# Optimization experiments

Measured on AMD Instinct MI355X. Metric: run time of the kernel, lower is better.

## Reference

```python
import jax, jax.numpy as jnp
import numpy as np

GAMMA = 0.9
TEMPERATURE = 0.07
BASE_TEMPERATURE = 0.07
U_SIZE = 15_000_000
BSZ, N_VIEWS, DIM = 2048, 2, 256


def setup_inputs() -> dict:
    key = jax.random.key(0)
    kf, = jax.random.split(key, 1)
    feats = jax.random.normal(kf, (BSZ, N_VIEWS, DIM), dtype=jnp.float32)
    # contrastive features are unit-normalized in practice
    feats = feats / jnp.linalg.norm(feats, axis=-1, keepdims=True)
    index = jnp.arange(BSZ, dtype=jnp.int64) if jax.config.jax_enable_x64 else jnp.arange(BSZ, dtype=jnp.int32)
    u = jnp.zeros((U_SIZE, 1), dtype=jnp.float32)
    return {"index": index, "features": feats, "u": u}


def reference(index, features, u):
    B, V, D = features.shape          # bsz, n_views, dim
    N = B * V
    eye_b = jnp.eye(B, dtype=jnp.float32)

    # torch.cat(torch.unbind(features, dim=1), dim=0) -> [V*B, D], views stacked
    contrast_feature = jnp.transpose(features, (1, 0, 2)).reshape(N, D)
    anchor_feature = contrast_feature  # contrast_mode == 'all'

    # [N, N] similarity logits
    anchor_dot_contrast = jnp.matmul(anchor_feature, contrast_feature.T) / TEMPERATURE
    logits_max = jax.lax.stop_gradient(jnp.max(anchor_dot_contrast, axis=1, keepdims=True))
    logits = anchor_dot_contrast - logits_max

    # positive mask: tiled identity with self-contrast removed
    mask = jnp.tile(eye_b, (V, V))
    logits_mask = 1.0 - jnp.eye(N, dtype=jnp.float32)  # scatter of zeros on the diagonal
    pos_mask = mask * logits_mask
    neg_mask = 1.0 - pos_mask

    # detached negative exp-logits (EMA statistics)
    neg_exp_logits = jax.lax.stop_gradient(jnp.exp(logits) * neg_mask)

    # indexed EMA buffer update: u[index] = (1-g)*u[index] + g*rowsum[:B]
    row_sum = jnp.sum(neg_exp_logits, axis=1, keepdims=True)[:B]   # [B, 1]
    u_new = (1.0 - GAMMA) * u[index] + GAMMA * row_sum             # [B, 1]
    # (buffer write: u = u.at[index].set(u_new); only u_new is read below)

    p_neg_pairs = neg_exp_logits / jnp.tile(u_new, (V, 1))         # [N, N], detached numer/denom
    log_prob = logits - jnp.sum(p_neg_pairs * logits * neg_mask, axis=1, keepdims=True)

    mean_log_prob_pos = jnp.sum(pos_mask * log_prob, axis=1) / jnp.sum(pos_mask, axis=1)
    loss = -(TEMPERATURE / BASE_TEMPERATURE) * mean_log_prob_pos
    return loss.reshape(V, B).mean()
```

## Files before the change

kernel.cpp:

```cpp
#include <hip/hip_runtime.h>


#define BSZ   2048
#define NROW  4096
#define DDIM  256
#define NB64  64
#define NT2   (NB64 * (NB64 + 1) / 2)
#define C1    (1.4426950408889634f / 0.07f)
#define LN2   0.6931471805599453f

typedef __attribute__((ext_vector_type(8))) __bf16 bf16x8;
typedef __attribute__((ext_vector_type(4))) float f32x4;

__device__ __forceinline__ short f2bs(float x) {
    __bf16 b = (__bf16)x;
    return __builtin_bit_cast(short, b);
}

__device__ __forceinline__ const float* crow_ptr(const float* feats, int i) {
    return feats + (((i & (BSZ - 1)) * 2 + (i >> 11)) << 8);
}

__global__ __launch_bounds__(256) void prep_kernel(const float* __restrict__ feats,
        float* __restrict__ Szero, short* __restrict__ CmF) {
    int gid = blockIdx.x * 256 + threadIdx.x;
    if (gid < 2 * NROW) Szero[gid] = 0.0f;

    int quad = gid & 3;
    int l15  = (gid >> 2) & 15;
    int rt   = (gid >> 6) & 3;
    int k    = (gid >> 8) & 7;
    int b    = gid >> 12;
    int srow = (b << 6) + (rt << 4) + l15;
    int kel  = (k << 5) + (quad << 3);
    const float4* fp = (const float4*)(crow_ptr(feats, srow) + kel);
    float4 v0 = fp[0], v1 = fp[1];
    short h[8] = { f2bs(v0.x), f2bs(v0.y), f2bs(v0.z), f2bs(v0.w),
                   f2bs(v1.x), f2bs(v1.y), f2bs(v1.z), f2bs(v1.w) };
    *(int4*)(CmF + gid * 8) = *(int4*)h;
}

__global__ __launch_bounds__(64, 3) void gemm_sym(const short* __restrict__ CmF,
        float* __restrict__ S1, float* __restrict__ S2,
        float* __restrict__ Praw, float* __restrict__ Draw) {
    int lane = threadIdx.x;
    int quad = lane >> 4;
    int l15  = lane & 15;

    int t = blockIdx.x;
    int p = (int)((sqrtf(8.0f * (float)t + 1.0f) - 1.0f) * 0.5f);
    while ((p + 1) * (p + 2) / 2 <= t) ++p;
    while (p * (p + 1) / 2 > t) --p;
    int q = t - p * (p + 1) / 2;
    int rowBase = q << 6;
    int colBase = p << 6;
    bool offdiag = (p != q);

    int laneOff = ((l15 << 2) + quad) * 8;
    int aO = q * 16384 + laneOff;
    int bO = p * 16384 + laneOff;

    f32x4 acc[4][4];
    #pragma unroll
    for (int a = 0; a < 4; ++a)
        #pragma unroll
        for (int c = 0; c < 4; ++c) acc[a][c] = (f32x4){0.f, 0.f, 0.f, 0.f};

    bf16x8 aF[2][4], bF[2][4];
    #pragma unroll
    for (int rt = 0; rt < 4; ++rt) {
        aF[0][rt] = *(const bf16x8*)(CmF + aO + rt * 512);
        bF[0][rt] = *(const bf16x8*)(CmF + bO + rt * 512);
    }

    #pragma unroll
    for (int k = 0; k < 8; ++k) {
        int cur = k & 1;
        int nxt = cur ^ 1;
        if (k < 7) {
            #pragma unroll
            for (int rt = 0; rt < 4; ++rt) {
                aF[nxt][rt] = *(const bf16x8*)(CmF + aO + ((k + 1) * 4 + rt) * 512);
                bF[nxt][rt] = *(const bf16x8*)(CmF + bO + ((k + 1) * 4 + rt) * 512);
            }
        }
        __builtin_amdgcn_s_setprio(1);
        #pragma unroll
        for (int rt = 0; rt < 4; ++rt)
            #pragma unroll
            for (int ct = 0; ct < 4; ++ct)
                acc[rt][ct] = __builtin_amdgcn_mfma_f32_16x16x32_bf16(
                    aF[cur][rt], bF[cur][ct], acc[rt][ct], 0, 0, 0);
        __builtin_amdgcn_s_setprio(0);
    }

    float S1r[4][4] = {}, S2r[4][4] = {};
    float S1c[4] = {}, S2c[4] = {};
    #pragma unroll
    for (int rt = 0; rt < 4; ++rt) {
        #pragma unroll
        for (int ct = 0; ct < 4; ++ct) {
            #pragma unroll
            for (int r = 0; r < 4; ++r) {
                float d  = acc[rt][ct][r];
                float t0 = d * C1;
                float f  = __builtin_exp2f(t0);
                S1r[rt][r] += f;
                S2r[rt][r] = __builtin_fmaf(f, t0, S2r[rt][r]);
                if (offdiag) {
                    S1c[ct] += f;
                    S2c[ct] = __builtin_fmaf(f, t0, S2c[ct]);
                }
            }
        }
    }

    if (p == (q ^ 32)) {
        if (quad == (l15 >> 2)) {
            int r = l15 & 3;
            #pragma unroll
            for (int rt = 0; rt < 4; ++rt) {
                float t0 = acc[rt][rt][r] * C1;
                Praw[rowBase + rt * 16 + l15] = t0;
                Praw[colBase + rt * 16 + l15] = t0;
            }
        }
    }
    if (!offdiag) {
        if (quad == (l15 >> 2)) {
            int r = l15 & 3;
            #pragma unroll
            for (int rt = 0; rt < 4; ++rt)
                Draw[rowBase + rt * 16 + l15] = acc[rt][rt][r] * C1;
        }
    }

    #pragma unroll
    for (int rt = 0; rt < 4; ++rt) {
        #pragma unroll
        for (int r = 0; r < 4; ++r) {
            float e = S1r[rt][r], w = S2r[rt][r];
            #pragma unroll
            for (int off = 1; off < 16; off <<= 1) {
                e += __shfl_xor(e, off, 64);
                w += __shfl_xor(w, off, 64);
            }
            if (l15 == 0) {
                int grow = rowBase + rt * 16 + (quad << 2) + r;
                atomicAdd(&S1[grow], e);
                atomicAdd(&S2[grow], w);
            }
        }
    }
    if (offdiag) {
        #pragma unroll
        for (int ct = 0; ct < 4; ++ct) {
            float e = S1c[ct], w = S2c[ct];
            e += __shfl_xor(e, 16, 64);  w += __shfl_xor(w, 16, 64);
            e += __shfl_xor(e, 32, 64);  w += __shfl_xor(w, 32, 64);
            if (quad == 0) {
                int gcol = colBase + ct * 16 + l15;
                atomicAdd(&S1[gcol], e);
                atomicAdd(&S2[gcol], w);
            }
        }
    }
}

__global__ __launch_bounds__(1024) void finalize_kernel(const int* __restrict__ index,
        const float* __restrict__ u, const float* __restrict__ S1,
        const float* __restrict__ S2, const float* __restrict__ Praw,
        const float* __restrict__ Draw, float* __restrict__ out) {
    __shared__ float unew[BSZ];
    __shared__ float partial[16];
    int tid = threadIdx.x;
    for (int b = tid; b < BSZ; b += 1024) {
        float m  = -Draw[b];
        float tp = Praw[b] + m;
        float E  = __builtin_exp2f(m) * S1[b];
        unew[b] = 0.1f * u[index[b]] + 0.9f * (E - __builtin_exp2f(tp));
    }
    __syncthreads();
    float local = 0.0f;
    for (int i = tid; i < NROW; i += 1024) {
        float m   = -Draw[i];
        float tp  = Praw[i] + m;
        float etp = __builtin_exp2f(tp);
        float W   = __builtin_exp2f(m) * __builtin_fmaf(m, S1[i], S2[i]);
        local += tp - (W - etp * tp) / unew[i & (BSZ - 1)];
    }
    #pragma unroll
    for (int off = 32; off; off >>= 1) local += __shfl_xor(local, off, 64);
    if ((tid & 63) == 0) partial[tid >> 6] = local;
    __syncthreads();
    if (tid == 0) {
        float s = 0.0f;
        #pragma unroll
        for (int w = 0; w < 16; ++w) s += partial[w];
        out[0] = -LN2 * s / (float)NROW;
    }
}

extern "C" void kernel_launch(void* const* d_in, const int* in_sizes, int n_in,
                              void* d_out, int out_size, void* d_ws, size_t ws_size,
                              hipStream_t stream) {
    const int*   index = (const int*)d_in[0];
    const float* feats = (const float*)d_in[1];
    const float* u     = (const float*)d_in[2];
    float* out = (float*)d_out;

    float* S1   = (float*)d_ws;
    float* S2   = S1 + NROW;
    float* Praw = S2 + NROW;
    float* Draw = Praw + NROW;
    short* CmF  = (short*)((char*)d_ws + 131072);

    prep_kernel<<<1024, 256, 0, stream>>>(feats, S1, CmF);
    gemm_sym<<<NT2, 64, 0, stream>>>(CmF, S1, S2, Praw, Draw);
    finalize_kernel<<<1, 1024, 0, stream>>>(index, u, S1, S2, Praw, Draw, out);
}
```

Before: 114.2 us.

## Triple-buffer GEMM fragment loads and parallelize finalize across blocks with atomics

The symmetric GEMM now prefetches two k-steps ahead with a three-slot register buffer instead of double buffering, and its launch-bounds occupancy hint drops from 3 to 2 to make room for the extra registers. The single-block 1024-thread finalize is replaced by 32 blocks of one wavefront each. Each block handles 64 paired rows and atomically adds into the output, which the prep kernel now zeroes. This aims to hide global load latency in the GEMM and shorten the serial finalize tail, at the cost of lower occupancy and a non-deterministic float atomic reduction order.

New measurement: 111.3 us, median of 2. 1.03x faster.

```diff
diff --git a/kernel.cpp b/kernel.cpp
--- a/kernel.cpp
+++ b/kernel.cpp
@@ -3,7 +3,6 @@
 
 #define BSZ   2048
 #define NROW  4096
-#define DDIM  256
 #define NB64  64
 #define NT2   (NB64 * (NB64 + 1) / 2)
 #define C1    (1.4426950408889634f / 0.07f)
@@ -21,11 +20,8 @@
     return feats + (((i & (BSZ - 1)) * 2 + (i >> 11)) << 8);
 }
 
-__global__ __launch_bounds__(256) void prep_kernel(const float* __restrict__ feats,
-        float* __restrict__ Szero, short* __restrict__ CmF) {
-    int gid = blockIdx.x * 256 + threadIdx.x;
-    if (gid < 2 * NROW) Szero[gid] = 0.0f;
-
+__device__ __forceinline__ void pack_unit(const float* __restrict__ feats,
+                                          short* __restrict__ CmF, int gid) {
     int quad = gid & 3;
     int l15  = (gid >> 2) & 15;
     int rt   = (gid >> 6) & 3;
@@ -40,7 +36,15 @@
     *(int4*)(CmF + gid * 8) = *(int4*)h;
 }
 
-__global__ __launch_bounds__(64, 3) void gemm_sym(const short* __restrict__ CmF,
+__global__ __launch_bounds__(256) void prep_kernel(const float* __restrict__ feats,
+        float* __restrict__ S1, short* __restrict__ CmF, float* __restrict__ out) {
+    int gid = blockIdx.x * 256 + threadIdx.x;
+    if (gid < 2 * NROW) S1[gid] = 0.0f;
+    else if (gid == 2 * NROW) out[0] = 0.0f;
+    pack_unit(feats, CmF, gid);
+}
+
+__global__ __launch_bounds__(64, 2) void gemm_sym(const short* __restrict__ CmF,
         float* __restrict__ S1, float* __restrict__ S2,
         float* __restrict__ Praw, float* __restrict__ Draw) {
     int lane = threadIdx.x;
@@ -57,8 +61,8 @@
     bool offdiag = (p != q);
 
     int laneOff = ((l15 << 2) + quad) * 8;
-    int aO = q * 16384 + laneOff;
-    int bO = p * 16384 + laneOff;
+    const short* aB = CmF + q * 16384 + laneOff;
+    const short* bB = CmF + p * 16384 + laneOff;
 
     f32x4 acc[4][4];
     #pragma unroll
@@ -66,22 +70,27 @@
         #pragma unroll
         for (int c = 0; c < 4; ++c) acc[a][c] = (f32x4){0.f, 0.f, 0.f, 0.f};
 
-    bf16x8 aF[2][4], bF[2][4];
-    #pragma unroll
-    for (int rt = 0; rt < 4; ++rt) {
-        aF[0][rt] = *(const bf16x8*)(CmF + aO + rt * 512);
-        bF[0][rt] = *(const bf16x8*)(CmF + bO + rt * 512);
+    bf16x8 aF[3][4], bF[3][4];
+    #pragma unroll
+    for (int rt = 0; rt < 4; ++rt) {
+        aF[0][rt] = *(const bf16x8*)(aB + (0 * 4 + rt) * 512);
+        bF[0][rt] = *(const bf16x8*)(bB + (0 * 4 + rt) * 512);
+    }
+    #pragma unroll
+    for (int rt = 0; rt < 4; ++rt) {
+        aF[1][rt] = *(const bf16x8*)(aB + (1 * 4 + rt) * 512);
+        bF[1][rt] = *(const bf16x8*)(bB + (1 * 4 + rt) * 512);
     }
 
     #pragma unroll
     for (int k = 0; k < 8; ++k) {
-        int cur = k & 1;
-        int nxt = cur ^ 1;
-        if (k < 7) {
+        int cur = k % 3;
+        int nxt = (k + 2) % 3;
+        if (k < 6) {
             #pragma unroll
             for (int rt = 0; rt < 4; ++rt) {
-                aF[nxt][rt] = *(const bf16x8*)(CmF + aO + ((k + 1) * 4 + rt) * 512);
-                bF[nxt][rt] = *(const bf16x8*)(CmF + bO + ((k + 1) * 4 + rt) * 512);
+                aF[nxt][rt] = *(const bf16x8*)(aB + ((k + 2) * 4 + rt) * 512);
+                bF[nxt][rt] = *(const bf16x8*)(bB + ((k + 2) * 4 + rt) * 512);
             }
         }
         __builtin_amdgcn_s_setprio(1);
@@ -115,24 +124,20 @@
         }
     }
 
-    if (p == (q ^ 32)) {
-        if (quad == (l15 >> 2)) {
-            int r = l15 & 3;
-            #pragma unroll
-            for (int rt = 0; rt < 4; ++rt) {
-                float t0 = acc[rt][rt][r] * C1;
-                Praw[rowBase + rt * 16 + l15] = t0;
-                Praw[colBase + rt * 16 + l15] = t0;
-            }
-        }
-    }
-    if (!offdiag) {
-        if (quad == (l15 >> 2)) {
-            int r = l15 & 3;
-            #pragma unroll
-            for (int rt = 0; rt < 4; ++rt)
-                Draw[rowBase + rt * 16 + l15] = acc[rt][rt][r] * C1;
-        }
+    if (p == (q ^ 32) && quad == (l15 >> 2)) {
+        int r = l15 & 3;
+        #pragma unroll
+        for (int rt = 0; rt < 4; ++rt) {
+            float t0 = acc[rt][rt][r] * C1;
+            Praw[rowBase + rt * 16 + l15] = t0;
+            Praw[colBase + rt * 16 + l15] = t0;
+        }
+    }
+    if (!offdiag && quad == (l15 >> 2)) {
+        int r = l15 & 3;
+        #pragma unroll
+        for (int rt = 0; rt < 4; ++rt)
+            Draw[rowBase + rt * 16 + l15] = acc[rt][rt][r] * C1;
     }
 
     #pragma unroll
@@ -167,38 +172,28 @@
     }
 }
 
-__global__ __launch_bounds__(1024) void finalize_kernel(const int* __restrict__ index,
+__global__ __launch_bounds__(64) void finalize_kernel(const int* __restrict__ index,
         const float* __restrict__ u, const float* __restrict__ S1,
         const float* __restrict__ S2, const float* __restrict__ Praw,
         const float* __restrict__ Draw, float* __restrict__ out) {
-    __shared__ float unew[BSZ];
-    __shared__ float partial[16];
-    int tid = threadIdx.x;
-    for (int b = tid; b < BSZ; b += 1024) {
-        float m  = -Draw[b];
-        float tp = Praw[b] + m;
-        float E  = __builtin_exp2f(m) * S1[b];
-        unew[b] = 0.1f * u[index[b]] + 0.9f * (E - __builtin_exp2f(tp));
-    }
-    __syncthreads();
-    float local = 0.0f;
-    for (int i = tid; i < NROW; i += 1024) {
-        float m   = -Draw[i];
-        float tp  = Praw[i] + m;
-        float etp = __builtin_exp2f(tp);
-        float W   = __builtin_exp2f(m) * __builtin_fmaf(m, S1[i], S2[i]);
-        local += tp - (W - etp * tp) / unew[i & (BSZ - 1)];
-    }
+    int lane = threadIdx.x;
+    int rlo  = (blockIdx.x << 6) + lane;
+    int rhi  = rlo + BSZ;
+
+    float mlo = -Draw[rlo], mhi = -Draw[rhi];
+    float tplo = Praw[rlo] + mlo, tphi = Praw[rhi] + mhi;
+    float Elo  = __builtin_exp2f(mlo) * S1[rlo];
+    float unew = 0.1f * u[index[rlo]] + 0.9f * (Elo - __builtin_exp2f(tplo));
+
+    float Wlo = __builtin_exp2f(mlo) * __builtin_fmaf(mlo, S1[rlo], S2[rlo]);
+    float Whi = __builtin_exp2f(mhi) * __builtin_fmaf(mhi, S1[rhi], S2[rhi]);
+    float etplo = __builtin_exp2f(tplo);
+    float etphi = __builtin_exp2f(tphi);
+    float local = (tplo - (Wlo - etplo * tplo) / unew)
+                + (tphi - (Whi - etphi * tphi) / unew);
     #pragma unroll
     for (int off = 32; off; off >>= 1) local += __shfl_xor(local, off, 64);
-    if ((tid & 63) == 0) partial[tid >> 6] = local;
-    __syncthreads();
-    if (tid == 0) {
-        float s = 0.0f;
-        #pragma unroll
-        for (int w = 0; w < 16; ++w) s += partial[w];
-        out[0] = -LN2 * s / (float)NROW;
-    }
+    if (lane == 0) atomicAdd(out, -LN2 * local / (float)NROW);
 }
 
 extern "C" void kernel_launch(void* const* d_in, const int* in_sizes, int n_in,
@@ -215,7 +210,7 @@
     float* Draw = Praw + NROW;
     short* CmF  = (short*)((char*)d_ws + 131072);
 
-    prep_kernel<<<1024, 256, 0, stream>>>(feats, S1, CmF);
+    prep_kernel<<<1024, 256, 0, stream>>>(feats, S1, CmF, out);
     gemm_sym<<<NT2, 64, 0, stream>>>(CmF, S1, S2, Praw, Draw);
-    finalize_kernel<<<1, 1024, 0, stream>>>(index, u, S1, S2, Praw, Draw, out);
-}
+    finalize_kernel<<<32, 64, 0, stream>>>(index, u, S1, S2, Praw, Draw, out);
+}
```
